# Optimization experiments

Measured on AMD Instinct MI355X. Metric: run time of the kernel, lower is better.

## Reference

```python
import jax, jax.numpy as jnp
import numpy as np

B, N, M, D = 8, 4096, 4096, 3

def setup_inputs() -> dict:
    key = jax.random.key(0)
    ks = jax.random.split(key, 6)
    return {
        "X_pred": jax.random.normal(ks[0], (B, N, D), dtype=jnp.float32),
        "X_true": jax.random.normal(ks[1], (B, M, D), dtype=jnp.float32),
        "R_pred": jax.random.normal(ks[2], (B, D, D), dtype=jnp.float32),
        "t_pred": jax.random.normal(ks[3], (B, D), dtype=jnp.float32),
        "R_true": jax.random.normal(ks[4], (B, D, D), dtype=jnp.float32),
        "t_true": jax.random.normal(ks[5], (B, D), dtype=jnp.float32),
        "temperature": jnp.asarray(0.1, dtype=jnp.float32),
    }

def reference(X_pred, X_true, R_pred, t_pred, R_true, t_true, temperature):
    # Rigid transforms: x' = R x + t
    Xp = jnp.einsum('bij,bnj->bni', R_pred, X_pred) + t_pred[:, None, :]  # (B,N,D)
    Xt = jnp.einsum('bij,bmj->bmi', R_true, X_true) + t_true[:, None, :]  # (B,M,D)
    # Squared pairwise distances: |a|^2 + |b|^2 - 2 a.b  (== cdist(p=2)**2)
    sq_p = jnp.sum(Xp * Xp, axis=-1)  # (B,N)
    sq_t = jnp.sum(Xt * Xt, axis=-1)  # (B,M)
    dist_sq = sq_p[:, :, None] + sq_t[:, None, :] - 2.0 * jnp.einsum('bnd,bmd->bnm', Xp, Xt)
    dist_sq = jnp.maximum(dist_sq, 0.0)  # (B,N,M)
    soft_alignment = jax.nn.softmax(-dist_sq / temperature, axis=-1)
    weighted_distances = jnp.sum(soft_alignment * dist_sq, axis=-1)  # (B,N)
    return jnp.mean(weighted_distances)
```

## Files before the change

kernel.cpp:

```cpp
#include <hip/hip_runtime.h>


#define B_    8
#define N_    4096
#define M_    4096
#define NWAVE 8
#define BLOCK 512
#define ROWS  512
#define RPL   8
#define MSPL  8
#define QCH   (M_ / MSPL)
#define WQ    (QCH / NWAVE)
#define LOG2E 1.4426950408889634f
#define LN2   0.6931471805599453f
#define BIGF  3.0e38f

__global__ __launch_bounds__(BLOCK, 4) void softfape_main(
    const float* __restrict__ X_pred, const float* __restrict__ X_true,
    const float* __restrict__ R_pred, const float* __restrict__ t_pred,
    const float* __restrict__ R_true, const float* __restrict__ t_true,
    const float* __restrict__ temp,
    float4* __restrict__ Pg)
{
    __shared__ float4 Q[QCH];
    __shared__ float  Mp[NWAVE][ROWS];
    __shared__ float  Lp[NWAVE][ROWS];
    __shared__ float  Sp[NWAVE][ROWS];
    __shared__ float  shl[ROWS];
    __shared__ float  pwl[ROWS];

    const int tid  = threadIdx.x;
    const int wave = tid >> 6;
    const int lane = tid & 63;
    const int x    = blockIdx.x;
    const int ms   = x & 7;
    const int rg   = (x >> 3) & 7;
    const int b    = x >> 6;

    const float T   = temp[0];
    const float c   = LOG2E / T;
    const float m2c = -2.0f * c;

    if (tid < QCH / 2) {
        const float g00 = R_true[b*9+0], g01 = R_true[b*9+1], g02 = R_true[b*9+2];
        const float g10 = R_true[b*9+3], g11 = R_true[b*9+4], g12 = R_true[b*9+5];
        const float g20 = R_true[b*9+6], g21 = R_true[b*9+7], g22 = R_true[b*9+8];
        const float u0  = t_true[b*3+0], u1 = t_true[b*3+1], u2 = t_true[b*3+2];
        const float2* xt = (const float2*)(X_true + ((size_t)b * M_ + ms * QCH) * 3);
        const float2 f0 = xt[3*tid+0], f1 = xt[3*tid+1], f2 = xt[3*tid+2];
        {
            const float y0 = fmaf(g00, f0.x, fmaf(g01, f0.y, fmaf(g02, f1.x, u0)));
            const float y1 = fmaf(g10, f0.x, fmaf(g11, f0.y, fmaf(g12, f1.x, u1)));
            const float y2 = fmaf(g20, f0.x, fmaf(g21, f0.y, fmaf(g22, f1.x, u2)));
            const float nn = fmaf(y0, y0, fmaf(y1, y1, y2 * y2));
            Q[2*tid]   = make_float4(m2c*y0, m2c*y1, m2c*y2, c*nn);
        }
        {
            const float y0 = fmaf(g00, f1.y, fmaf(g01, f2.x, fmaf(g02, f2.y, u0)));
            const float y1 = fmaf(g10, f1.y, fmaf(g11, f2.x, fmaf(g12, f2.y, u1)));
            const float y2 = fmaf(g20, f1.y, fmaf(g21, f2.x, fmaf(g22, f2.y, u2)));
            const float nn = fmaf(y0, y0, fmaf(y1, y1, y2 * y2));
            Q[2*tid+1] = make_float4(m2c*y0, m2c*y1, m2c*y2, c*nn);
        }
    }

    float px[RPL], py[RPL], pz[RPL];
    {
        const float h00 = R_pred[b*9+0], h01 = R_pred[b*9+1], h02 = R_pred[b*9+2];
        const float h10 = R_pred[b*9+3], h11 = R_pred[b*9+4], h12 = R_pred[b*9+5];
        const float h20 = R_pred[b*9+6], h21 = R_pred[b*9+7], h22 = R_pred[b*9+8];
        const float v0 = t_pred[b*3+0], v1 = t_pred[b*3+1], v2 = t_pred[b*3+2];
        const float4* xp = (const float4*)(X_pred + ((size_t)b * N_ + rg * ROWS + lane * RPL) * 3);
        float f[24];
        #pragma unroll
        for (int i = 0; i < 6; ++i) *(float4*)&f[4*i] = xp[i];
        #pragma unroll
        for (int r = 0; r < RPL; ++r) {
            const float rx = f[3*r], ry = f[3*r+1], rz = f[3*r+2];
            px[r] = fmaf(h00, rx, fmaf(h01, ry, fmaf(h02, rz, v0)));
            py[r] = fmaf(h10, rx, fmaf(h11, ry, fmaf(h12, rz, v1)));
            pz[r] = fmaf(h20, rx, fmaf(h21, ry, fmaf(h22, rz, v2)));
            const float pw = c * fmaf(px[r], px[r], fmaf(py[r], py[r], pz[r] * pz[r]));
            pwl[RPL*lane + r] = pw;
        }
    }

    __syncthreads();

    const float4* __restrict__ Qw = Q + wave * WQ;

    float mA[RPL];
    #pragma unroll
    for (int r = 0; r < RPL; ++r) mA[r] = BIGF;
    for (int k0 = 0; k0 < WQ; k0 += 8) {
        float4 qv[8];
        #pragma unroll
        for (int j = 0; j < 8; ++j) qv[j] = Qw[k0 + j];
        #pragma unroll
        for (int j2 = 0; j2 < 4; ++j2) {
            const float4 q0 = qv[2*j2], q1 = qv[2*j2+1];
            #pragma unroll
            for (int r = 0; r < RPL; ++r) {
                const float A0 = fmaf(q0.x, px[r], fmaf(q0.y, py[r], fmaf(q0.z, pz[r], q0.w)));
                const float A1 = fmaf(q1.x, px[r], fmaf(q1.y, py[r], fmaf(q1.z, pz[r], q1.w)));
                mA[r] = fminf(mA[r], fminf(A0, A1));
            }
        }
    }
    *(float4*)&Mp[wave][RPL*lane]     = make_float4(mA[0], mA[1], mA[2], mA[3]);
    *(float4*)&Mp[wave][RPL*lane + 4] = make_float4(mA[4], mA[5], mA[6], mA[7]);
    __syncthreads();

    {
        float m = Mp[0][tid];
        #pragma unroll
        for (int w2 = 1; w2 < NWAVE; ++w2) m = fminf(m, Mp[w2][tid]);
        shl[tid] = m;
    }
    __syncthreads();

    float sh[RPL];
    {
        const float4 s0 = *(const float4*)&shl[RPL*lane];
        const float4 s1 = *(const float4*)&shl[RPL*lane + 4];
        sh[0]=s0.x; sh[1]=s0.y; sh[2]=s0.z; sh[3]=s0.w;
        sh[4]=s1.x; sh[5]=s1.y; sh[6]=s1.z; sh[7]=s1.w;
    }

    float L[RPL], S[RPL];
    #pragma unroll
    for (int r = 0; r < RPL; ++r) { L[r] = 0.0f; S[r] = 0.0f; }
    for (int k0 = 0; k0 < WQ; k0 += 8) {
        float4 qv[8];
        #pragma unroll
        for (int j = 0; j < 8; ++j) qv[j] = Qw[k0 + j];
        #pragma unroll
        for (int j = 0; j < 8; ++j) {
            const float4 q = qv[j];
            #pragma unroll
            for (int r = 0; r < RPL; ++r) {
                const float A   = fmaf(q.x, px[r], fmaf(q.y, py[r], fmaf(q.z, pz[r], q.w)));
                const float arg = shl ? (sh[r] - A) : 0.0f;
                const float w   = __builtin_amdgcn_exp2f(sh[r] - A);
                L[r] += w;
                (void)arg;
                S[r] = fmaf(w, sh[r] - A, S[r]);
            }
        }
    }
    *(float4*)&Lp[wave][RPL*lane]     = make_float4(L[0], L[1], L[2], L[3]);
    *(float4*)&Lp[wave][RPL*lane + 4] = make_float4(L[4], L[5], L[6], L[7]);
    *(float4*)&Sp[wave][RPL*lane]     = make_float4(S[0], S[1], S[2], S[3]);
    *(float4*)&Sp[wave][RPL*lane + 4] = make_float4(S[4], S[5], S[6], S[7]);
    __syncthreads();

    {
        float Lr = 0.0f, Sr = 0.0f;
        #pragma unroll
        for (int w2 = 0; w2 < NWAVE; ++w2) { Lr += Lp[w2][tid]; Sr += Sp[w2][tid]; }
        const size_t row = (size_t)b * N_ + rg * ROWS + tid;
        Pg[row * MSPL + ms] = make_float4(shl[tid] + pwl[tid], Lr, Sr, 0.0f);
    }
}

__global__ __launch_bounds__(256) void softfape_finalize(
    const float4* __restrict__ Pg, const float* __restrict__ temp,
    float* __restrict__ out)
{
    __shared__ float ws4[4];
    const int tid = threadIdx.x;
    const size_t row = (size_t)blockIdx.x * 256 + tid;

    float4 P[MSPL];
    #pragma unroll
    for (int i = 0; i < MSPL; ++i) P[i] = Pg[row * MSPL + i];

    float m = P[0].x;
    #pragma unroll
    for (int i = 1; i < MSPL; ++i) m = fminf(m, P[i].x);

    float L = 0.0f, SA = 0.0f;
    #pragma unroll
    for (int i = 0; i < MSPL; ++i) {
        const float dm = m - P[i].x;
        const float f  = __builtin_amdgcn_exp2f(dm);
        L  = fmaf(P[i].y, f, L);
        SA = fmaf(f, fmaf(dm, P[i].y, P[i].z), SA);
    }
    float wd = m - SA / L;

    wd += __shfl_xor(wd, 1);  wd += __shfl_xor(wd, 2);  wd += __shfl_xor(wd, 4);
    wd += __shfl_xor(wd, 8);  wd += __shfl_xor(wd, 16); wd += __shfl_xor(wd, 32);
    if ((tid & 63) == 0) ws4[tid >> 6] = wd;
    __syncthreads();
    if (tid == 0) {
        const float s = ws4[0] + ws4[1] + ws4[2] + ws4[3];
        const float scale = temp[0] * LN2 / ((float)B_ * (float)N_);
        atomicAdd(out, s * scale);
    }
}

extern "C" void kernel_launch(void* const* d_in, const int* in_sizes, int n_in,
                              void* d_out, int out_size, void* d_ws, size_t ws_size,
                              hipStream_t stream) {
    const float* X_pred = (const float*)d_in[0];
    const float* X_true = (const float*)d_in[1];
    const float* R_pred = (const float*)d_in[2];
    const float* t_pred = (const float*)d_in[3];
    const float* R_true = (const float*)d_in[4];
    const float* t_true = (const float*)d_in[5];
    const float* temp   = (const float*)d_in[6];
    float* out = (float*)d_out;

    float4* Pg = (float4*)d_ws;

    hipMemsetAsync(out, 0, sizeof(float), stream);

    softfape_main<<<dim3(B_ * (N_ / ROWS) * MSPL), BLOCK, 0, stream>>>(
        X_pred, X_true, R_pred, t_pred, R_true, t_true, temp, Pg);

    softfape_finalize<<<dim3((B_ * N_) / 256), 256, 0, stream>>>(Pg, temp, out);
}
```

Measured before the change: 103.7 us.

## Fuse max and exp-sum passes using an analytic softmax shift

Removes the separate min-reduction pass over all targets. Each row's exp2 shift becomes -c*|p|^2, which keeps every exponent argument at or below zero, so one pass now accumulates the sum, the weighted sum and a running max. The finalize kernel falls back to the maximum argument, i.e. the nearest distance, when every weight underflows to zero. This halves the sweeps over the target points and drops two block barriers. The cost is accuracy: rows whose closest points are far away can lose precision or underflow entirely.

Result: faster. 95.75 us (-7.7%).

```diff
diff --git a/kernel.cpp b/kernel.cpp
--- a/kernel.cpp
+++ b/kernel.cpp
@@ -13,7 +13,7 @@
 #define WQ    (QCH / NWAVE)
 #define LOG2E 1.4426950408889634f
 #define LN2   0.6931471805599453f
-#define BIGF  3.0e38f
+#define NEGBIG -3.0e38f
 
 __global__ __launch_bounds__(BLOCK, 4) void softfape_main(
     const float* __restrict__ X_pred, const float* __restrict__ X_true,
@@ -23,11 +23,9 @@
     float4* __restrict__ Pg)
 {
     __shared__ float4 Q[QCH];
-    __shared__ float  Mp[NWAVE][ROWS];
     __shared__ float  Lp[NWAVE][ROWS];
     __shared__ float  Sp[NWAVE][ROWS];
-    __shared__ float  shl[ROWS];
-    __shared__ float  pwl[ROWS];
+    __shared__ float  Mp[NWAVE][ROWS];
 
     const int tid  = threadIdx.x;
     const int wave = tid >> 6;
@@ -64,7 +62,7 @@
         }
     }
 
-    float px[RPL], py[RPL], pz[RPL];
+    float px[RPL], py[RPL], pz[RPL], sh[RPL];
     {
         const float h00 = R_pred[b*9+0], h01 = R_pred[b*9+1], h02 = R_pred[b*9+2];
         const float h10 = R_pred[b*9+3], h11 = R_pred[b*9+4], h12 = R_pred[b*9+5];
@@ -80,8 +78,7 @@
             px[r] = fmaf(h00, rx, fmaf(h01, ry, fmaf(h02, rz, v0)));
             py[r] = fmaf(h10, rx, fmaf(h11, ry, fmaf(h12, rz, v1)));
             pz[r] = fmaf(h20, rx, fmaf(h21, ry, fmaf(h22, rz, v2)));
-            const float pw = c * fmaf(px[r], px[r], fmaf(py[r], py[r], pz[r] * pz[r]));
-            pwl[RPL*lane + r] = pw;
+            sh[r] = -c * fmaf(px[r], px[r], fmaf(py[r], py[r], pz[r] * pz[r]));
         }
     }
 
@@ -89,9 +86,9 @@
 
     const float4* __restrict__ Qw = Q + wave * WQ;
 
-    float mA[RPL];
+    float L[RPL], S[RPL], mx[RPL];
     #pragma unroll
-    for (int r = 0; r < RPL; ++r) mA[r] = BIGF;
+    for (int r = 0; r < RPL; ++r) { L[r] = 0.0f; S[r] = 0.0f; mx[r] = NEGBIG; }
     for (int k0 = 0; k0 < WQ; k0 += 8) {
         float4 qv[8];
         #pragma unroll
@@ -101,50 +98,17 @@
             const float4 q0 = qv[2*j2], q1 = qv[2*j2+1];
             #pragma unroll
             for (int r = 0; r < RPL; ++r) {
-                const float A0 = fmaf(q0.x, px[r], fmaf(q0.y, py[r], fmaf(q0.z, pz[r], q0.w)));
-                const float A1 = fmaf(q1.x, px[r], fmaf(q1.y, py[r], fmaf(q1.z, pz[r], q1.w)));
-                mA[r] = fminf(mA[r], fminf(A0, A1));
-            }
-        }
-    }
-    *(float4*)&Mp[wave][RPL*lane]     = make_float4(mA[0], mA[1], mA[2], mA[3]);
-    *(float4*)&Mp[wave][RPL*lane + 4] = make_float4(mA[4], mA[5], mA[6], mA[7]);
-    __syncthreads();
-
-    {
-        float m = Mp[0][tid];
-        #pragma unroll
-        for (int w2 = 1; w2 < NWAVE; ++w2) m = fminf(m, Mp[w2][tid]);
-        shl[tid] = m;
-    }
-    __syncthreads();
-
-    float sh[RPL];
-    {
-        const float4 s0 = *(const float4*)&shl[RPL*lane];
-        const float4 s1 = *(const float4*)&shl[RPL*lane + 4];
-        sh[0]=s0.x; sh[1]=s0.y; sh[2]=s0.z; sh[3]=s0.w;
-        sh[4]=s1.x; sh[5]=s1.y; sh[6]=s1.z; sh[7]=s1.w;
-    }
-
-    float L[RPL], S[RPL];
-    #pragma unroll
-    for (int r = 0; r < RPL; ++r) { L[r] = 0.0f; S[r] = 0.0f; }
-    for (int k0 = 0; k0 < WQ; k0 += 8) {
-        float4 qv[8];
-        #pragma unroll
-        for (int j = 0; j < 8; ++j) qv[j] = Qw[k0 + j];
-        #pragma unroll
-        for (int j = 0; j < 8; ++j) {
-            const float4 q = qv[j];
-            #pragma unroll
-            for (int r = 0; r < RPL; ++r) {
-                const float A   = fmaf(q.x, px[r], fmaf(q.y, py[r], fmaf(q.z, pz[r], q.w)));
-                const float arg = shl ? (sh[r] - A) : 0.0f;
-                const float w   = __builtin_amdgcn_exp2f(sh[r] - A);
-                L[r] += w;
-                (void)arg;
-                S[r] = fmaf(w, sh[r] - A, S[r]);
+                const float A0   = fmaf(q0.x, px[r], fmaf(q0.y, py[r], fmaf(q0.z, pz[r], q0.w)));
+                const float A1   = fmaf(q1.x, px[r], fmaf(q1.y, py[r], fmaf(q1.z, pz[r], q1.w)));
+                const float arg0 = sh[r] - A0;
+                const float arg1 = sh[r] - A1;
+                const float w0   = __builtin_amdgcn_exp2f(arg0);
+                const float w1   = __builtin_amdgcn_exp2f(arg1);
+                L[r] += w0;
+                L[r] += w1;
+                S[r]  = fmaf(w0, arg0, S[r]);
+                S[r]  = fmaf(w1, arg1, S[r]);
+                mx[r] = fmaxf(fmaxf(mx[r], arg0), arg1);
             }
         }
     }
@@ -152,14 +116,18 @@
     *(float4*)&Lp[wave][RPL*lane + 4] = make_float4(L[4], L[5], L[6], L[7]);
     *(float4*)&Sp[wave][RPL*lane]     = make_float4(S[0], S[1], S[2], S[3]);
     *(float4*)&Sp[wave][RPL*lane + 4] = make_float4(S[4], S[5], S[6], S[7]);
+    *(float4*)&Mp[wave][RPL*lane]     = make_float4(mx[0], mx[1], mx[2], mx[3]);
+    *(float4*)&Mp[wave][RPL*lane + 4] = make_float4(mx[4], mx[5], mx[6], mx[7]);
     __syncthreads();
 
     {
-        float Lr = 0.0f, Sr = 0.0f;
+        float Lr = 0.0f, Sr = 0.0f, mw = Mp[0][tid];
         #pragma unroll
         for (int w2 = 0; w2 < NWAVE; ++w2) { Lr += Lp[w2][tid]; Sr += Sp[w2][tid]; }
+        #pragma unroll
+        for (int w2 = 1; w2 < NWAVE; ++w2) mw = fmaxf(mw, Mp[w2][tid]);
         const size_t row = (size_t)b * N_ + rg * ROWS + tid;
-        Pg[row * MSPL + ms] = make_float4(shl[tid] + pwl[tid], Lr, Sr, 0.0f);
+        Pg[row * MSPL + ms] = make_float4(0.0f, Lr, Sr, mw);
     }
 }
 
@@ -176,8 +144,9 @@
     for (int i = 0; i < MSPL; ++i) P[i] = Pg[row * MSPL + i];
 
     float m = P[0].x;
+    float mw = P[0].w;
     #pragma unroll
-    for (int i = 1; i < MSPL; ++i) m = fminf(m, P[i].x);
+    for (int i = 1; i < MSPL; ++i) { m = fminf(m, P[i].x); mw = fmaxf(mw, P[i].w); }
 
     float L = 0.0f, SA = 0.0f;
     #pragma unroll
@@ -187,7 +156,7 @@
         L  = fmaf(P[i].y, f, L);
         SA = fmaf(f, fmaf(dm, P[i].y, P[i].z), SA);
     }
-    float wd = m - SA / L;
+    float wd = (L > 0.0f) ? (m - SA / L) : -mw;
 
     wd += __shfl_xor(wd, 1);  wd += __shfl_xor(wd, 2);  wd += __shfl_xor(wd, 4);
     wd += __shfl_xor(wd, 8);  wd += __shfl_xor(wd, 16); wd += __shfl_xor(wd, 32);
```
